# Kernel tuning notes

Measured on AMD Instinct MI355X. Metric: run time of the kernel, lower is better.

The kernel has to match this reference:

```python
import jax, jax.numpy as jnp
import numpy as np

LSH_NUM_PROJS = 7
BLOCK_SIZE = 256      # key block size
SAMPLE_SIZE = 256
B, H, N, D = 1, 32, 8192, 128


def _gray_perm(num_projs):
    # AngularLSH._unit_hamming_distance_array: Gray-code bucket permutation
    a = np.array([0, 1], dtype=np.int32)
    for _ in range(num_projs - 1):
        a = np.concatenate([a, np.flip(a) + a.shape[0]])
    return jnp.asarray(a)


def _lsh_hash(x, proj_dir, perm):
    # x: [B,H,N,D], proj_dir: [D,R] -> bucket ids [B,H,N]
    bits = jnp.einsum('bhnd,dr->bhnr', x, proj_dir) > 0
    enc = 2 ** jnp.arange(proj_dir.shape[-1], dtype=jnp.int32)
    bin_ids = jnp.sum(bits.astype(jnp.int32) * enc, axis=-1)
    return perm[bin_ids]


def _attn_lse(q, k, v, scale, bias=None):
    # exact attention returning output and log-sum-exp of scaled scores
    s = jnp.einsum('...qd,...kd->...qk', q, k) * scale
    if bias is not None:
        s = s + bias
    m = jnp.max(s, axis=-1, keepdims=True)
    p = jnp.exp(s - m)
    denom = jnp.sum(p, axis=-1, keepdims=True)
    attn = jnp.einsum('...qk,...kd->...qd', p, v) / denom
    lse = m + jnp.log(denom)  # [..., q, 1]
    return attn, lse


def _take(x, idx):
    # gather along the sequence axis (dim 2); idx: [B,H,M]
    return jnp.take_along_axis(x, idx[..., None], axis=2)


def hyper_attention(q, k, v, proj_dir, sampled_set):
    b, h, n, d = q.shape
    scale = d ** -0.5
    perm = _gray_perm(LSH_NUM_PROJS)
    # 1) sortLSH: sort q and k by angular-LSH bucket (stable)
    q_idx = jnp.argsort(_lsh_hash(q, proj_dir, perm), axis=2)
    k_idx = jnp.argsort(_lsh_hash(k, proj_dir, perm), axis=2)
    q_idx_inv = jnp.argsort(q_idx, axis=2)
    q_s = _take(q, q_idx)
    k_s = _take(k, k_idx)
    v_s = _take(v, k_idx)
    nb = n // BLOCK_SIZE          # number of key blocks
    qbs = n // nb                 # query block size
    # block-diagonal exact attention in sorted order
    qb = q_s.reshape(b, h, nb, qbs, d)
    kb = k_s.reshape(b, h, nb, BLOCK_SIZE, d)
    vb = v_s.reshape(b, h, nb, BLOCK_SIZE, d)
    attn_blk, lse_blk = _attn_lse(qb, kb, vb, scale)
    attn_blk = attn_blk.reshape(b, h, n, d)
    lse_blk = lse_blk.reshape(b, h, n, 1)
    attn_blk = _take(attn_blk, q_idx_inv)
    lse_blk = _take(lse_blk, q_idx_inv)
    # 2) residual: uniform sampling of keys (indices into sorted key order)
    s_size = sampled_set.shape[-1]
    k_sub = _take(k_s, sampled_set)   # [B,H,S,D]
    v_sub = _take(v_s, sampled_set)
    # mask out samples falling in the query's own diagonal block
    same_block = (jnp.arange(n)[None, None, :, None] // qbs) == (sampled_set[:, :, None, :] // BLOCK_SIZE)
    bias = jnp.where(same_block, jnp.finfo(q.dtype).min, 0.0).astype(q.dtype)
    attn_res, lse_res = _attn_lse(q_s, k_sub, v_sub, scale, bias=bias)
    lse_res = lse_res + jnp.log(n / s_size)  # importance weight n_key/sample_size
    attn_res = _take(attn_res, q_idx_inv)
    lse_res = _take(lse_res, q_idx_inv)
    # 3) combine estimators: softmax-weighted average in log space
    lse = jnp.logaddexp(lse_blk, lse_res)
    return jnp.exp(lse_blk - lse) * attn_blk + jnp.exp(lse_res - lse) * attn_res


def setup_inputs() -> dict:
    key = jax.random.key(0)
    k1, k2, k3, k4, k5 = jax.random.split(key, 5)
    return {
        'queries': jax.random.normal(k1, (B, H, N, D), dtype=jnp.float32),
        'keys': jax.random.normal(k2, (B, H, N, D), dtype=jnp.float32),
        'vals': jax.random.normal(k3, (B, H, N, D), dtype=jnp.float32),
        'proj_dir': jax.random.normal(k4, (D, LSH_NUM_PROJS), dtype=jnp.float32),
        'sampled_set': jax.random.randint(k5, (B, H, SAMPLE_SIZE), 0, N),
    }


def reference(queries, keys, vals, proj_dir, sampled_set):
    return hyper_attention(queries, keys, vals, proj_dir, sampled_set)
```

## Files before the change

kernel.cpp:

```cpp
#include <hip/hip_runtime.h>
#include <hip/hip_bf16.h>
#include <math.h>

#define Hh 32
#define Nseq 8192
#define Dh 128
#define NBd 32
#define BLKSZ 256
#define SAMP 256
#define KVT 512
#define CHK 64
#define NCH 8
#define LOG32 3.4657359027997265f
#define SCALE 0.088388347648318447f
#define SKW 136

typedef float f32x4 __attribute__((ext_vector_type(4)));
typedef unsigned ui32x4 __attribute__((ext_vector_type(4)));
typedef __bf16 bf16x8 __attribute__((ext_vector_type(8)));

__device__ __forceinline__ f32x4 mfma16(bf16x8 a, bf16x8 b, f32x4 c) {
  return __builtin_amdgcn_mfma_f32_16x16x32_bf16(a, b, c, 0, 0, 0);
}

__device__ __forceinline__ bf16x8 cvt8(const float* __restrict__ p) {
  float4 a = ((const float4*)p)[0];
  float4 b = ((const float4*)p)[1];
  bf16x8 r;
  r[0] = (__bf16)a.x; r[1] = (__bf16)a.y; r[2] = (__bf16)a.z; r[3] = (__bf16)a.w;
  r[4] = (__bf16)b.x; r[5] = (__bf16)b.y; r[6] = (__bf16)b.z; r[7] = (__bf16)b.w;
  return r;
}

__device__ __forceinline__ bf16x8 cvt8v(float4 a, float4 b) {
  bf16x8 r;
  r[0] = (__bf16)a.x; r[1] = (__bf16)a.y; r[2] = (__bf16)a.z; r[3] = (__bf16)a.w;
  r[4] = (__bf16)b.x; r[5] = (__bf16)b.y; r[6] = (__bf16)b.z; r[7] = (__bf16)b.w;
  return r;
}

__device__ __forceinline__ unsigned pack2(float a, float b, float& ra, float& rb) {
  __bf16 ba = (__bf16)a, bb = (__bf16)b;
  ra = (float)ba; rb = (float)bb;
  return ((unsigned)__builtin_bit_cast(unsigned short, bb) << 16) |
         (unsigned)__builtin_bit_cast(unsigned short, ba);
}

__global__ __launch_bounds__(256) void lsh_hash_kernel(
    const float* __restrict__ q, const float* __restrict__ k,
    const float* __restrict__ proj, int* __restrict__ buckets) {
  int row = blockIdx.x * 256 + threadIdx.x;
  const float* x = ((row >> 18) ? k : q) + (size_t)(row & (Hh * Nseq - 1)) * Dh;
  double acc[7] = {0, 0, 0, 0, 0, 0, 0};
#pragma unroll 8
  for (int d0 = 0; d0 < Dh; d0 += 4) {
    float4 xv = *(const float4*)(x + d0);
    double x0 = (double)xv.x, x1 = (double)xv.y, x2 = (double)xv.z, x3 = (double)xv.w;
#pragma unroll
    for (int j = 0; j < 7; j++) {
      acc[j] = fma(x0, (double)proj[(d0 + 0) * 7 + j], acc[j]);
      acc[j] = fma(x1, (double)proj[(d0 + 1) * 7 + j], acc[j]);
      acc[j] = fma(x2, (double)proj[(d0 + 2) * 7 + j], acc[j]);
      acc[j] = fma(x3, (double)proj[(d0 + 3) * 7 + j], acc[j]);
    }
  }
  int bin = 0;
#pragma unroll
  for (int j = 0; j < 7; j++) bin |= (acc[j] > 0.0 ? 1 : 0) << j;
  buckets[row] = bin ^ (bin >> 1);
}

__global__ __launch_bounds__(64) void bucket_sort_kernel(
    const int* __restrict__ buckets, int* __restrict__ idx) {
  __shared__ unsigned hist[64][128];
  int t = threadIdx.x;
  int base = blockIdx.x * Nseq;
  for (int b = 0; b < 128; b++) hist[t][b] = 0;
  __syncthreads();
  for (int i = 0; i < 128; i++) {
    int b = buckets[base + t * 128 + i];
    hist[t][b]++;
  }
  __syncthreads();
  int b0 = 2 * t, b1 = 2 * t + 1;
  unsigned tot0 = 0, tot1 = 0;
  for (int tt = 0; tt < 64; tt++) { unsigned h = hist[tt][b0]; hist[tt][b0] = tot0; tot0 += h; }
  for (int tt = 0; tt < 64; tt++) { unsigned h = hist[tt][b1]; hist[tt][b1] = tot1; tot1 += h; }
  unsigned pair = tot0 + tot1;
  unsigned scan = pair;
  for (int s = 1; s < 64; s <<= 1) {
    unsigned u = __shfl_up(scan, s);
    if (t >= s) scan += u;
  }
  unsigned start0 = scan - pair;
  unsigned start1 = start0 + tot0;
  __syncthreads();
  for (int tt = 0; tt < 64; tt++) { hist[tt][b0] += start0; hist[tt][b1] += start1; }
  __syncthreads();
  for (int i = 0; i < 128; i++) {
    int gi = t * 128 + i;
    int b = buckets[base + gi];
    unsigned pos = hist[t][b]++;
    idx[base + pos] = gi;
  }
}

__global__ __launch_bounds__(512, 2) void hyper_attn_kernel(
    const float* __restrict__ q, const float* __restrict__ k, const float* __restrict__ v,
    const int* __restrict__ sampled, const int* __restrict__ q_idx,
    const int* __restrict__ k_idx, float* __restrict__ out) {
  __shared__ int s_orig[KVT];
  __shared__ __attribute__((aligned(16))) float s_add[KVT];
  __shared__ __attribute__((aligned(16))) __bf16 s_k[2][CHK][SKW];
  __shared__ __attribute__((aligned(16))) __bf16 s_vt[2][Dh][72];

  const int c = blockIdx.x, bh = blockIdx.y;
  const int tid = threadIdx.x;
  const int w = tid >> 6, l = tid & 63;
  const int l4 = l >> 4, lm = l & 15;
  const int jk = tid >> 3, pk = tid & 7;

  {
    int jj = tid;
    if (jj < BLKSZ) {
      s_orig[jj] = k_idx[bh * Nseq + c * BLKSZ + jj];
      s_add[jj] = 0.0f;
    } else {
      int sp = sampled[bh * SAMP + (jj - BLKSZ)];
      s_orig[jj] = k_idx[bh * Nseq + sp];
      s_add[jj] = ((sp >> 8) == c) ? -1e38f : LOG32;
    }
  }

  bf16x8 qf[2][4];
  const int* qi = q_idx + bh * Nseq + c * BLKSZ + w * 32;
#pragma unroll
  for (int rt = 0; rt < 2; rt++) {
    int orig = qi[rt * 16 + lm];
    const float* qp = q + ((size_t)bh * Nseq + orig) * Dh + l4 * 8;
#pragma unroll
    for (int dc = 0; dc < 4; dc++) qf[rt][dc] = cvt8(qp + dc * 32);
  }

  f32x4 O[2][8];
  float mrow[2] = {-INFINITY, -INFINITY};
  float lsum[2] = {0.f, 0.f};
#pragma unroll
  for (int rt = 0; rt < 2; rt++)
#pragma unroll
    for (int dt = 0; dt < 8; dt++) { O[rt][dt][0]=0.f; O[rt][dt][1]=0.f; O[rt][dt][2]=0.f; O[rt][dt][3]=0.f; }

  __syncthreads();

  {
    int origk = s_orig[jk];
    const float* kp = k + ((size_t)bh * Nseq + origk) * Dh + pk * 16;
    *(bf16x8*)&s_k[0][jk][pk * 16]     = cvt8(kp);
    *(bf16x8*)&s_k[0][jk][pk * 16 + 8] = cvt8(kp + 8);
    int origv = s_orig[l];
    const float* vp = v + ((size_t)bh * Nseq + origv) * Dh + w * 16;
    float4 A = ((const float4*)vp)[0], B = ((const float4*)vp)[1];
    float4 C = ((const float4*)vp)[2], Dv = ((const float4*)vp)[3];
    float tmp[16] = {A.x,A.y,A.z,A.w,B.x,B.y,B.z,B.w,C.x,C.y,C.z,C.w,Dv.x,Dv.y,Dv.z,Dv.w};
#pragma unroll
    for (int dd = 0; dd < 16; dd++) s_vt[0][w * 16 + dd][l] = (__bf16)tmp[dd];
  }
  __syncthreads();

  const int laneA = lm + 32 * (l4 & 1);
  const bool hi = (l4 >> 1) & 1;

  for (int ch = 0; ch < NCH; ch++) {
    const int cur = ch & 1;
    const bool pf = (ch + 1 < NCH);

    float4 kA, kB, kC, kD, vA, vB, vC, vD;
    if (pf) {
      int origk = s_orig[(ch + 1) * CHK + jk];
      const float4* kp = (const float4*)(k + ((size_t)bh * Nseq + origk) * Dh + pk * 16);
      kA = kp[0]; kB = kp[1]; kC = kp[2]; kD = kp[3];
      int origv = s_orig[(ch + 1) * CHK + l];
      const float4* vp = (const float4*)(v + ((size_t)bh * Nseq + origv) * Dh + w * 16);
      vA = vp[0]; vB = vp[1]; vC = vp[2]; vD = vp[3];
    }

    float sc[2][4][4];
#pragma unroll
    for (int ct = 0; ct < 4; ct++) {
      f32x4 acc0, acc1;
      acc0[0]=0.f;acc0[1]=0.f;acc0[2]=0.f;acc0[3]=0.f;
      acc1[0]=0.f;acc1[1]=0.f;acc1[2]=0.f;acc1[3]=0.f;
#pragma unroll
      for (int dc = 0; dc < 4; dc++) {
        bf16x8 kf = *(const bf16x8*)&s_k[cur][ct * 16 + lm][dc * 32 + l4 * 8];
        acc0 = mfma16(kf, qf[0][dc], acc0);
        acc1 = mfma16(kf, qf[1][dc], acc1);
      }
      f32x4 addv = *(const f32x4*)&s_add[ch * CHK + ct * 16 + l4 * 4];
#pragma unroll
      for (int r = 0; r < 4; r++) {
        sc[0][ct][r] = acc0[r] * SCALE + addv[r];
        sc[1][ct][r] = acc1[r] * SCALE + addv[r];
      }
    }

    unsigned q01[2][4], q23[2][4];
#pragma unroll
    for (int rt = 0; rt < 2; rt++) {
      float mc = sc[rt][0][0];
#pragma unroll
      for (int ct = 0; ct < 4; ct++)
#pragma unroll
        for (int r = 0; r < 4; r++) mc = fmaxf(mc, sc[rt][ct][r]);
      mc = fmaxf(mc, __shfl_xor(mc, 16));
      mc = fmaxf(mc, __shfl_xor(mc, 32));
      float mn = fmaxf(mrow[rt], mc);
      float alpha = __expf(mrow[rt] - mn);
      mrow[rt] = mn;
      f32x4 aO;
#pragma unroll
      for (int r = 0; r < 4; r++) aO[r] = __shfl(alpha, l4 * 4 + r);
#pragma unroll
      for (int dt = 0; dt < 8; dt++) O[rt][dt] *= aO;
      float rsum = 0.f;
#pragma unroll
      for (int ct = 0; ct < 4; ct++) {
        float p0 = __expf(sc[rt][ct][0] - mn);
        float p1 = __expf(sc[rt][ct][1] - mn);
        float p2 = __expf(sc[rt][ct][2] - mn);
        float p3 = __expf(sc[rt][ct][3] - mn);
        float ra, rb, rc, rd;
        q01[rt][ct] = pack2(p0, p1, ra, rb);
        q23[rt][ct] = pack2(p2, p3, rc, rd);
        rsum += (ra + rb) + (rc + rd);
      }
      rsum += __shfl_xor(rsum, 16);
      rsum += __shfl_xor(rsum, 32);
      lsum[rt] = lsum[rt] * alpha + rsum;
    }

    if (pf) {
      *(bf16x8*)&s_k[cur ^ 1][jk][pk * 16]     = cvt8v(kA, kB);
      *(bf16x8*)&s_k[cur ^ 1][jk][pk * 16 + 8] = cvt8v(kC, kD);
      float tmp[16] = {vA.x,vA.y,vA.z,vA.w,vB.x,vB.y,vB.z,vB.w,
                       vC.x,vC.y,vC.z,vC.w,vD.x,vD.y,vD.z,vD.w};
#pragma unroll
      for (int dd = 0; dd < 16; dd++) s_vt[cur ^ 1][w * 16 + dd][l] = (__bf16)tmp[dd];
    }

#pragma unroll
    for (int kc = 0; kc < 2; kc++) {
      bf16x8 pa[2];
#pragma unroll
      for (int rt = 0; rt < 2; rt++) {
        unsigned a0 = __shfl((int)q01[rt][2 * kc],     laneA);
        unsigned b0 = __shfl((int)q01[rt][2 * kc + 1], laneA);
        unsigned a1 = __shfl((int)q23[rt][2 * kc],     laneA);
        unsigned b1 = __shfl((int)q23[rt][2 * kc + 1], laneA);
        unsigned a2 = __shfl((int)q01[rt][2 * kc],     laneA + 16);
        unsigned b2 = __shfl((int)q01[rt][2 * kc + 1], laneA + 16);
        unsigned a3 = __shfl((int)q23[rt][2 * kc],     laneA + 16);
        unsigned b3 = __shfl((int)q23[rt][2 * kc + 1], laneA + 16);
        ui32x4 pw;
        pw[0] = hi ? b0 : a0;
        pw[1] = hi ? b1 : a1;
        pw[2] = hi ? b2 : a2;
        pw[3] = hi ? b3 : a3;
        pa[rt] = __builtin_bit_cast(bf16x8, pw);
      }
#pragma unroll
      for (int dt = 0; dt < 8; dt++) {
        bf16x8 vb = *(const bf16x8*)&s_vt[cur][dt * 16 + lm][kc * 32 + l4 * 8];
        O[0][dt] = mfma16(pa[0], vb, O[0][dt]);
        O[1][dt] = mfma16(pa[1], vb, O[1][dt]);
      }
    }
    __syncthreads();
  }

#pragma unroll
  for (int rt = 0; rt < 2; rt++) {
    float inv = 1.0f / lsum[rt];
    f32x4 invr;
#pragma unroll
    for (int r = 0; r < 4; r++) invr[r] = __shfl(inv, l4 * 4 + r);
    int orow[4];
#pragma unroll
    for (int r = 0; r < 4; r++)
      orow[r] = q_idx[bh * Nseq + c * BLKSZ + w * 32 + rt * 16 + l4 * 4 + r];
#pragma unroll
    for (int r = 0; r < 4; r++) {
      float* op = out + ((size_t)bh * Nseq + orow[r]) * Dh + lm;
#pragma unroll
      for (int dt = 0; dt < 8; dt++) op[dt * 16] = O[rt][dt][r] * invr[r];
    }
  }
}

extern "C" void kernel_launch(void* const* d_in, const int* in_sizes, int n_in,
                              void* d_out, int out_size, void* d_ws, size_t ws_size,
                              hipStream_t stream) {
  const float* q    = (const float*)d_in[0];
  const float* k    = (const float*)d_in[1];
  const float* v    = (const float*)d_in[2];
  const float* proj = (const float*)d_in[3];
  const int* samp   = (const int*)d_in[4];
  float* out = (float*)d_out;

  int* buckets = (int*)d_ws;
  int* idx = buckets + 2 * Hh * Nseq;

  lsh_hash_kernel<<<(2 * Hh * Nseq) / 256, 256, 0, stream>>>(q, k, proj, buckets);
  bucket_sort_kernel<<<2 * Hh, 64, 0, stream>>>(buckets, idx);
  hyper_attn_kernel<<<dim3(NBd, Hh), 512, 0, stream>>>(
      q, k, v, samp, idx , idx + Hh * Nseq , out);
}
```

Measured before the change: 274.2 us.

## Remap V transpose stores to paired 32-bit writes and swizzle block order

```diff
diff --git a/kernel.cpp b/kernel.cpp
--- a/kernel.cpp
+++ b/kernel.cpp
@@ -39,6 +39,12 @@
   return r;
 }
 
+__device__ __forceinline__ unsigned packv(float a, float b) {
+  __bf16 ba = (__bf16)a, bb = (__bf16)b;
+  return ((unsigned)__builtin_bit_cast(unsigned short, bb) << 16) |
+         (unsigned)__builtin_bit_cast(unsigned short, ba);
+}
+
 __device__ __forceinline__ unsigned pack2(float a, float b, float& ra, float& rb) {
   __bf16 ba = (__bf16)a, bb = (__bf16)b;
   ra = (float)ba; rb = (float)bb;
@@ -114,11 +120,13 @@
   __shared__ __attribute__((aligned(16))) __bf16 s_k[2][CHK][SKW];
   __shared__ __attribute__((aligned(16))) __bf16 s_vt[2][Dh][72];
 
-  const int c = blockIdx.x, bh = blockIdx.y;
+  const int swz = ((blockIdx.x & 7) << 7) | (blockIdx.x >> 3);
+  const int c = swz & 31, bh = swz >> 5;
   const int tid = threadIdx.x;
   const int w = tid >> 6, l = tid & 63;
   const int l4 = l >> 4, lm = l & 15;
   const int jk = tid >> 3, pk = tid & 7;
+  const int kb = (tid & 31) * 2, dg = tid >> 5;
 
   {
     int jj = tid;
@@ -157,13 +165,15 @@
     const float* kp = k + ((size_t)bh * Nseq + origk) * Dh + pk * 16;
     *(bf16x8*)&s_k[0][jk][pk * 16]     = cvt8(kp);
     *(bf16x8*)&s_k[0][jk][pk * 16 + 8] = cvt8(kp + 8);
-    int origv = s_orig[l];
-    const float* vp = v + ((size_t)bh * Nseq + origv) * Dh + w * 16;
-    float4 A = ((const float4*)vp)[0], B = ((const float4*)vp)[1];
-    float4 C = ((const float4*)vp)[2], Dv = ((const float4*)vp)[3];
-    float tmp[16] = {A.x,A.y,A.z,A.w,B.x,B.y,B.z,B.w,C.x,C.y,C.z,C.w,Dv.x,Dv.y,Dv.z,Dv.w};
-#pragma unroll
-    for (int dd = 0; dd < 16; dd++) s_vt[0][w * 16 + dd][l] = (__bf16)tmp[dd];
+    int ra = s_orig[kb], rb = s_orig[kb + 1];
+    const float4* va = (const float4*)(v + ((size_t)bh * Nseq + ra) * Dh + dg * 8);
+    const float4* vb = (const float4*)(v + ((size_t)bh * Nseq + rb) * Dh + dg * 8);
+    float4 A0 = va[0], A1 = va[1], B0 = vb[0], B1 = vb[1];
+    float ta[8] = {A0.x,A0.y,A0.z,A0.w,A1.x,A1.y,A1.z,A1.w};
+    float tb[8] = {B0.x,B0.y,B0.z,B0.w,B1.x,B1.y,B1.z,B1.w};
+#pragma unroll
+    for (int dd = 0; dd < 8; dd++)
+      *(unsigned*)&s_vt[0][dg * 8 + dd][kb] = packv(ta[dd], tb[dd]);
   }
   __syncthreads();
 
@@ -174,15 +184,17 @@
     const int cur = ch & 1;
     const bool pf = (ch + 1 < NCH);
 
-    float4 kA, kB, kC, kD, vA, vB, vC, vD;
+    float4 kA, kB, kC, kD, vA0, vA1, vB0, vB1;
     if (pf) {
       int origk = s_orig[(ch + 1) * CHK + jk];
       const float4* kp = (const float4*)(k + ((size_t)bh * Nseq + origk) * Dh + pk * 16);
       kA = kp[0]; kB = kp[1]; kC = kp[2]; kD = kp[3];
-      int origv = s_orig[(ch + 1) * CHK + l];
-      const float4* vp = (const float4*)(v + ((size_t)bh * Nseq + origv) * Dh + w * 16);
-      vA = vp[0]; vB = vp[1]; vC = vp[2]; vD = vp[3];
-    }
+      int ra = s_orig[(ch + 1) * CHK + kb], rb = s_orig[(ch + 1) * CHK + kb + 1];
+      const float4* va = (const float4*)(v + ((size_t)bh * Nseq + ra) * Dh + dg * 8);
+      const float4* vb = (const float4*)(v + ((size_t)bh * Nseq + rb) * Dh + dg * 8);
+      vA0 = va[0]; vA1 = va[1]; vB0 = vb[0]; vB1 = vb[1];
+    }
+    __builtin_amdgcn_sched_barrier(0);
 
     float sc[2][4][4];
 #pragma unroll
@@ -242,10 +254,11 @@
     if (pf) {
       *(bf16x8*)&s_k[cur ^ 1][jk][pk * 16]     = cvt8v(kA, kB);
       *(bf16x8*)&s_k[cur ^ 1][jk][pk * 16 + 8] = cvt8v(kC, kD);
-      float tmp[16] = {vA.x,vA.y,vA.z,vA.w,vB.x,vB.y,vB.z,vB.w,
-                       vC.x,vC.y,vC.z,vC.w,vD.x,vD.y,vD.z,vD.w};
-#pragma unroll
-      for (int dd = 0; dd < 16; dd++) s_vt[cur ^ 1][w * 16 + dd][l] = (__bf16)tmp[dd];
+      float ta[8] = {vA0.x,vA0.y,vA0.z,vA0.w,vA1.x,vA1.y,vA1.z,vA1.w};
+      float tb[8] = {vB0.x,vB0.y,vB0.z,vB0.w,vB1.x,vB1.y,vB1.z,vB1.w};
+#pragma unroll
+      for (int dd = 0; dd < 8; dd++)
+        *(unsigned*)&s_vt[cur ^ 1][dg * 8 + dd][kb] = packv(ta[dd], tb[dd]);
     }
 
 #pragma unroll
@@ -312,6 +325,6 @@
 
   lsh_hash_kernel<<<(2 * Hh * Nseq) / 256, 256, 0, stream>>>(q, k, proj, buckets);
   bucket_sort_kernel<<<2 * Hh, 64, 0, stream>>>(buckets, idx);
-  hyper_attn_kernel<<<dim3(NBd, Hh), 512, 0, stream>>>(
+  hyper_attn_kernel<<<NBd * Hh, 512, 0, stream>>>(
       q, k, v, samp, idx , idx + Hh * Nseq , out);
 }
```

After: 279.3 us. About the same (+1.9%).

## Split block and residual attention into two kernels with shared sampled KV

Applied to the files above, without the earlier changes.

```diff
diff --git a/kernel.cpp b/kernel.cpp
--- a/kernel.cpp
+++ b/kernel.cpp
@@ -8,12 +8,11 @@
 #define NBd 32
 #define BLKSZ 256
 #define SAMP 256
-#define KVT 512
 #define CHK 64
-#define NCH 8
 #define LOG32 3.4657359027997265f
 #define SCALE 0.088388347648318447f
 #define SKW 136
+#define SVB 264
 
 typedef float f32x4 __attribute__((ext_vector_type(4)));
 typedef unsigned ui32x4 __attribute__((ext_vector_type(4)));
@@ -105,12 +104,11 @@
   }
 }
 
-__global__ __launch_bounds__(512, 2) void hyper_attn_kernel(
+__global__ __launch_bounds__(512, 2) void hyper_attn_blk_kernel(
     const float* __restrict__ q, const float* __restrict__ k, const float* __restrict__ v,
-    const int* __restrict__ sampled, const int* __restrict__ q_idx,
-    const int* __restrict__ k_idx, float* __restrict__ out) {
-  __shared__ int s_orig[KVT];
-  __shared__ __attribute__((aligned(16))) float s_add[KVT];
+    const int* __restrict__ q_idx, const int* __restrict__ k_idx,
+    float* __restrict__ out, float* __restrict__ lse_ws) {
+  __shared__ int s_orig[BLKSZ];
   __shared__ __attribute__((aligned(16))) __bf16 s_k[2][CHK][SKW];
   __shared__ __attribute__((aligned(16))) __bf16 s_vt[2][Dh][72];
 
@@ -120,17 +118,7 @@
   const int l4 = l >> 4, lm = l & 15;
   const int jk = tid >> 3, pk = tid & 7;
 
-  {
-    int jj = tid;
-    if (jj < BLKSZ) {
-      s_orig[jj] = k_idx[bh * Nseq + c * BLKSZ + jj];
-      s_add[jj] = 0.0f;
-    } else {
-      int sp = sampled[bh * SAMP + (jj - BLKSZ)];
-      s_orig[jj] = k_idx[bh * Nseq + sp];
-      s_add[jj] = ((sp >> 8) == c) ? -1e38f : LOG32;
-    }
-  }
+  if (tid < BLKSZ) s_orig[tid] = k_idx[bh * Nseq + c * BLKSZ + tid];
 
   bf16x8 qf[2][4];
   const int* qi = q_idx + bh * Nseq + c * BLKSZ + w * 32;
@@ -170,9 +158,9 @@
   const int laneA = lm + 32 * (l4 & 1);
   const bool hi = (l4 >> 1) & 1;
 
-  for (int ch = 0; ch < NCH; ch++) {
+  for (int ch = 0; ch < 4; ch++) {
     const int cur = ch & 1;
-    const bool pf = (ch + 1 < NCH);
+    const bool pf = (ch + 1 < 4);
 
     float4 kA, kB, kC, kD, vA, vB, vC, vD;
     if (pf) {
@@ -196,11 +184,10 @@
         acc0 = mfma16(kf, qf[0][dc], acc0);
         acc1 = mfma16(kf, qf[1][dc], acc1);
       }
-      f32x4 addv = *(const f32x4*)&s_add[ch * CHK + ct * 16 + l4 * 4];
 #pragma unroll
       for (int r = 0; r < 4; r++) {
-        sc[0][ct][r] = acc0[r] * SCALE + addv[r];
-        sc[1][ct][r] = acc1[r] * SCALE + addv[r];
+        sc[0][ct][r] = acc0[r] * SCALE;
+        sc[1][ct][r] = acc1[r] * SCALE;
       }
     }
 
@@ -242,10 +229,10 @@
     if (pf) {
       *(bf16x8*)&s_k[cur ^ 1][jk][pk * 16]     = cvt8v(kA, kB);
       *(bf16x8*)&s_k[cur ^ 1][jk][pk * 16 + 8] = cvt8v(kC, kD);
-      float tmp[16] = {vA.x,vA.y,vA.z,vA.w,vB.x,vB.y,vB.z,vB.w,
-                       vC.x,vC.y,vC.z,vC.w,vD.x,vD.y,vD.z,vD.w};
-#pragma unroll
-      for (int dd = 0; dd < 16; dd++) s_vt[cur ^ 1][w * 16 + dd][l] = (__bf16)tmp[dd];
+      float ta[16] = {vA.x,vA.y,vA.z,vA.w,vB.x,vB.y,vB.z,vB.w,
+                      vC.x,vC.y,vC.z,vC.w,vD.x,vD.y,vD.z,vD.w};
+#pragma unroll
+      for (int dd = 0; dd < 16; dd++) s_vt[cur ^ 1][w * 16 + dd][l] = (__bf16)ta[dd];
     }
 
 #pragma unroll
@@ -294,6 +281,182 @@
 #pragma unroll
       for (int dt = 0; dt < 8; dt++) op[dt * 16] = O[rt][dt][r] * invr[r];
     }
+    if (l4 == 0) {
+      int orow0 = q_idx[bh * Nseq + c * BLKSZ + w * 32 + rt * 16 + lm];
+      lse_ws[bh * Nseq + orow0] = mrow[rt] + __logf(lsum[rt]);
+    }
+  }
+}
+
+__global__ __launch_bounds__(512, 1) void hyper_attn_res_kernel(
+    const float* __restrict__ q, const float* __restrict__ k, const float* __restrict__ v,
+    const int* __restrict__ sampled, const int* __restrict__ q_idx,
+    const int* __restrict__ k_idx, const float* __restrict__ lse_ws,
+    float* __restrict__ out) {
+  __shared__ int s_sp[SAMP];
+  __shared__ __attribute__((aligned(16))) __bf16 s_k[SAMP][SKW];
+  __shared__ __attribute__((aligned(16))) __bf16 s_vt[Dh][SVB];
+
+  const int bh = blockIdx.x >> 3, oct = blockIdx.x & 7;
+  const int tid = threadIdx.x;
+  const int w = tid >> 6, l = tid & 63;
+  const int l4 = l >> 4, lm = l & 15;
+  const int jk = tid >> 3, pk = tid & 7;
+
+  if (tid < SAMP) s_sp[tid] = sampled[bh * SAMP + tid];
+
+#pragma unroll
+  for (int ps = 0; ps < 4; ps++) {
+    int key = ps * 64 + jk;
+    int sp = sampled[bh * SAMP + key];
+    int orig = k_idx[bh * Nseq + sp];
+    const float4* kp = (const float4*)(k + ((size_t)bh * Nseq + orig) * Dh + pk * 16);
+    *(bf16x8*)&s_k[key][pk * 16]     = cvt8v(kp[0], kp[1]);
+    *(bf16x8*)&s_k[key][pk * 16 + 8] = cvt8v(kp[2], kp[3]);
+  }
+#pragma unroll
+  for (int ps = 0; ps < 4; ps++) {
+    int key = ps * 64 + l;
+    int sp = sampled[bh * SAMP + key];
+    int orig = k_idx[bh * Nseq + sp];
+    const float4* vp = (const float4*)(v + ((size_t)bh * Nseq + orig) * Dh + w * 16);
+    float4 A = vp[0], B = vp[1], C = vp[2], Dv = vp[3];
+    float tmp[16] = {A.x,A.y,A.z,A.w,B.x,B.y,B.z,B.w,C.x,C.y,C.z,C.w,Dv.x,Dv.y,Dv.z,Dv.w};
+#pragma unroll
+    for (int dd = 0; dd < 16; dd++) s_vt[w * 16 + dd][key] = (__bf16)tmp[dd];
+  }
+  __syncthreads();
+
+  const int laneA = lm + 32 * (l4 & 1);
+  const bool hi = (l4 >> 1) & 1;
+
+  for (int t = 0; t < 4; t++) {
+    const int rowb = oct * 1024 + w * 128 + t * 32;
+    const int c_tile = rowb >> 8;
+
+    bf16x8 qf[2][4];
+#pragma unroll
+    for (int rt = 0; rt < 2; rt++) {
+      int orig = q_idx[bh * Nseq + rowb + rt * 16 + lm];
+      const float* qp = q + ((size_t)bh * Nseq + orig) * Dh + l4 * 8;
+#pragma unroll
+      for (int dc = 0; dc < 4; dc++) qf[rt][dc] = cvt8(qp + dc * 32);
+    }
+
+    f32x4 O[2][8];
+    float mrow[2] = {-INFINITY, -INFINITY};
+    float lsum[2] = {0.f, 0.f};
+#pragma unroll
+    for (int rt = 0; rt < 2; rt++)
+#pragma unroll
+      for (int dt = 0; dt < 8; dt++) { O[rt][dt][0]=0.f; O[rt][dt][1]=0.f; O[rt][dt][2]=0.f; O[rt][dt][3]=0.f; }
+
+    for (int ch = 0; ch < 4; ch++) {
+      float sc[2][4][4];
+#pragma unroll
+      for (int ct = 0; ct < 4; ct++) {
+        f32x4 acc0, acc1;
+        acc0[0]=0.f;acc0[1]=0.f;acc0[2]=0.f;acc0[3]=0.f;
+        acc1[0]=0.f;acc1[1]=0.f;acc1[2]=0.f;acc1[3]=0.f;
+#pragma unroll
+        for (int dc = 0; dc < 4; dc++) {
+          bf16x8 kf = *(const bf16x8*)&s_k[ch * 64 + ct * 16 + lm][dc * 32 + l4 * 8];
+          acc0 = mfma16(kf, qf[0][dc], acc0);
+          acc1 = mfma16(kf, qf[1][dc], acc1);
+        }
+        ui32x4 spv = *(const ui32x4*)&s_sp[ch * 64 + ct * 16 + l4 * 4];
+#pragma unroll
+        for (int r = 0; r < 4; r++) {
+          float add = ((((int)spv[r]) >> 8) == c_tile) ? -1e38f : LOG32;
+          sc[0][ct][r] = acc0[r] * SCALE + add;
+          sc[1][ct][r] = acc1[r] * SCALE + add;
+        }
+      }
+
+      unsigned q01[2][4], q23[2][4];
+#pragma unroll
+      for (int rt = 0; rt < 2; rt++) {
+        float mc = sc[rt][0][0];
+#pragma unroll
+        for (int ct = 0; ct < 4; ct++)
+#pragma unroll
+          for (int r = 0; r < 4; r++) mc = fmaxf(mc, sc[rt][ct][r]);
+        mc = fmaxf(mc, __shfl_xor(mc, 16));
+        mc = fmaxf(mc, __shfl_xor(mc, 32));
+        float mn = fmaxf(mrow[rt], mc);
+        float alpha = __expf(mrow[rt] - mn);
+        mrow[rt] = mn;
+        f32x4 aO;
+#pragma unroll
+        for (int r = 0; r < 4; r++) aO[r] = __shfl(alpha, l4 * 4 + r);
+#pragma unroll
+        for (int dt = 0; dt < 8; dt++) O[rt][dt] *= aO;
+        float rsum = 0.f;
+#pragma unroll
+        for (int ct = 0; ct < 4; ct++) {
+          float p0 = __expf(sc[rt][ct][0] - mn);
+          float p1 = __expf(sc[rt][ct][1] - mn);
+          float p2 = __expf(sc[rt][ct][2] - mn);
+          float p3 = __expf(sc[rt][ct][3] - mn);
+          float ra, rb, rc, rd;
+          q01[rt][ct] = pack2(p0, p1, ra, rb);
+          q23[rt][ct] = pack2(p2, p3, rc, rd);
+          rsum += (ra + rb) + (rc + rd);
+        }
+        rsum += __shfl_xor(rsum, 16);
+        rsum += __shfl_xor(rsum, 32);
+        lsum[rt] = lsum[rt] * alpha + rsum;
+      }
+
+#pragma unroll
+      for (int kc = 0; kc < 2; kc++) {
+        bf16x8 pa[2];
+#pragma unroll
+        for (int rt = 0; rt < 2; rt++) {
+          unsigned a0 = __shfl((int)q01[rt][2 * kc],     laneA);
+          unsigned b0 = __shfl((int)q01[rt][2 * kc + 1], laneA);
+          unsigned a1 = __shfl((int)q23[rt][2 * kc],     laneA);
+          unsigned b1 = __shfl((int)q23[rt][2 * kc + 1], laneA);
+          unsigned a2 = __shfl((int)q01[rt][2 * kc],     laneA + 16);
+          unsigned b2 = __shfl((int)q01[rt][2 * kc + 1], laneA + 16);
+          unsigned a3 = __shfl((int)q23[rt][2 * kc],     laneA + 16);
+          unsigned b3 = __shfl((int)q23[rt][2 * kc + 1], laneA + 16);
+          ui32x4 pw;
+          pw[0] = hi ? b0 : a0;
+          pw[1] = hi ? b1 : a1;
+          pw[2] = hi ? b2 : a2;
+          pw[3] = hi ? b3 : a3;
+          pa[rt] = __builtin_bit_cast(bf16x8, pw);
+        }
+#pragma unroll
+        for (int dt = 0; dt < 8; dt++) {
+          bf16x8 vb = *(const bf16x8*)&s_vt[dt * 16 + lm][ch * 64 + kc * 32 + l4 * 8];
+          O[0][dt] = mfma16(pa[0], vb, O[0][dt]);
+          O[1][dt] = mfma16(pa[1], vb, O[1][dt]);
+        }
+      }
+    }
+
+#pragma unroll
+    for (int rt = 0; rt < 2; rt++) {
+      float lse_r = mrow[rt] + __logf(lsum[rt]);
+      float inv = 1.0f / lsum[rt];
+#pragma unroll
+      for (int r = 0; r < 4; r++) {
+        float lrr  = __shfl(lse_r, l4 * 4 + r);
+        float invr = __shfl(inv,   l4 * 4 + r);
+        int orow = q_idx[bh * Nseq + rowb + rt * 16 + l4 * 4 + r];
+        float lb = lse_ws[bh * Nseq + orow];
+        float m2 = fmaxf(lb, lrr);
+        float wb = __expf(lb - m2), wr = __expf(lrr - m2);
+        float sw = 1.0f / (wb + wr);
+        wb *= sw; wr *= sw;
+        float* op = out + ((size_t)bh * Nseq + orow) * Dh + lm;
+#pragma unroll
+        for (int dt = 0; dt < 8; dt++)
+          op[dt * 16] = wb * op[dt * 16] + wr * (O[rt][dt][r] * invr);
+      }
+    }
   }
 }
 
@@ -309,9 +472,12 @@
 
   int* buckets = (int*)d_ws;
   int* idx = buckets + 2 * Hh * Nseq;
+  float* lse_ws = (float*)buckets;
 
   lsh_hash_kernel<<<(2 * Hh * Nseq) / 256, 256, 0, stream>>>(q, k, proj, buckets);
   bucket_sort_kernel<<<2 * Hh, 64, 0, stream>>>(buckets, idx);
-  hyper_attn_kernel<<<dim3(NBd, Hh), 512, 0, stream>>>(
-      q, k, v, samp, idx , idx + Hh * Nseq , out);
-}
+  hyper_attn_blk_kernel<<<dim3(NBd, Hh), 512, 0, stream>>>(
+      q, k, v, idx , idx + Hh * Nseq , out, lse_ws);
+  hyper_attn_res_kernel<<<8 * Hh, 512, 0, stream>>>(
+      q, k, v, samp, idx , idx + Hh * Nseq , lse_ws, out);
+}
```

Result: slower. 326.3 us (+19.0%).

## Precompute sampled K/V in bf16 with pre-transposed V in a separate kernel

Applied to the files above, without the earlier changes.

```diff
diff --git a/kernel.cpp b/kernel.cpp
--- a/kernel.cpp
+++ b/kernel.cpp
@@ -8,12 +8,12 @@
 #define NBd 32
 #define BLKSZ 256
 #define SAMP 256
-#define KVT 512
 #define CHK 64
 #define NCH 8
 #define LOG32 3.4657359027997265f
 #define SCALE 0.088388347648318447f
 #define SKW 136
+#define SVW 72
 
 typedef float f32x4 __attribute__((ext_vector_type(4)));
 typedef unsigned ui32x4 __attribute__((ext_vector_type(4)));
@@ -105,30 +105,68 @@
   }
 }
 
+__global__ __launch_bounds__(256) void permute_samp_kernel(
+    const float* __restrict__ k, const float* __restrict__ v,
+    const int* __restrict__ k_idx, const int* __restrict__ sampled,
+    __bf16* __restrict__ K_sp, __bf16* __restrict__ V_sp) {
+  __shared__ __attribute__((aligned(16))) __bf16 s_t[Dh][SVW];
+  const int tile = blockIdx.x, bh = blockIdx.y;
+  const int t = threadIdx.x;
+  const int j = t >> 2, seg = (t & 3) * 32;
+  const int dpos = tile * 64 + j;
+  const int sp = sampled[bh * SAMP + dpos];
+  const int orig = k_idx[bh * Nseq + sp];
+  {
+    const float4* kp = (const float4*)(k + ((size_t)bh * Nseq + orig) * Dh + seg);
+    __bf16* dst = K_sp + ((size_t)bh * SAMP + dpos) * Dh + seg;
+#pragma unroll
+    for (int i = 0; i < 4; i++) *(bf16x8*)(dst + i * 8) = cvt8v(kp[2 * i], kp[2 * i + 1]);
+  }
+  {
+    const float4* vp = (const float4*)(v + ((size_t)bh * Nseq + orig) * Dh + seg);
+#pragma unroll
+    for (int i = 0; i < 8; i++) {
+      float4 a = vp[i];
+      s_t[seg + i * 4 + 0][j] = (__bf16)a.x;
+      s_t[seg + i * 4 + 1][j] = (__bf16)a.y;
+      s_t[seg + i * 4 + 2][j] = (__bf16)a.z;
+      s_t[seg + i * 4 + 3][j] = (__bf16)a.w;
+    }
+  }
+  __syncthreads();
+  {
+    int d = t >> 1, half = (t & 1) * 32;
+    __bf16* dst = V_sp + ((size_t)(bh * Dh + d)) * SAMP + tile * 64 + half;
+    const __bf16* srcp = &s_t[d][half];
+#pragma unroll
+    for (int i = 0; i < 4; i++) *(ui32x4*)(dst + i * 8) = *(const ui32x4*)(srcp + i * 8);
+  }
+}
+
 __global__ __launch_bounds__(512, 2) void hyper_attn_kernel(
     const float* __restrict__ q, const float* __restrict__ k, const float* __restrict__ v,
+    const __bf16* __restrict__ K_sp, const __bf16* __restrict__ V_sp,
     const int* __restrict__ sampled, const int* __restrict__ q_idx,
     const int* __restrict__ k_idx, float* __restrict__ out) {
-  __shared__ int s_orig[KVT];
-  __shared__ __attribute__((aligned(16))) float s_add[KVT];
+  __shared__ int s_orig[BLKSZ];
+  __shared__ __attribute__((aligned(16))) float s_add[SAMP];
   __shared__ __attribute__((aligned(16))) __bf16 s_k[2][CHK][SKW];
-  __shared__ __attribute__((aligned(16))) __bf16 s_vt[2][Dh][72];
+  __shared__ __attribute__((aligned(16))) __bf16 s_vt[2][Dh][SVW];
 
   const int c = blockIdx.x, bh = blockIdx.y;
   const int tid = threadIdx.x;
   const int w = tid >> 6, l = tid & 63;
   const int l4 = l >> 4, lm = l & 15;
   const int jk = tid >> 3, pk = tid & 7;
+  const int dv = tid >> 2, ks = (tid & 3) * 16;
 
   {
     int jj = tid;
     if (jj < BLKSZ) {
       s_orig[jj] = k_idx[bh * Nseq + c * BLKSZ + jj];
-      s_add[jj] = 0.0f;
     } else {
       int sp = sampled[bh * SAMP + (jj - BLKSZ)];
-      s_orig[jj] = k_idx[bh * Nseq + sp];
-      s_add[jj] = ((sp >> 8) == c) ? -1e38f : LOG32;
+      s_add[jj - BLKSZ] = ((sp >> 8) == c) ? -1e38f : LOG32;
     }
   }
 
@@ -172,16 +210,24 @@
 
   for (int ch = 0; ch < NCH; ch++) {
     const int cur = ch & 1;
-    const bool pf = (ch + 1 < NCH);
+    const int cn = ch + 1;
+    const bool pfg = (cn < 4);
+    const bool pfc = (cn >= 4 && cn < NCH);
 
     float4 kA, kB, kC, kD, vA, vB, vC, vD;
-    if (pf) {
-      int origk = s_orig[(ch + 1) * CHK + jk];
+    ui32x4 ksA, ksB, vsA, vsB;
+    if (pfg) {
+      int origk = s_orig[cn * CHK + jk];
       const float4* kp = (const float4*)(k + ((size_t)bh * Nseq + origk) * Dh + pk * 16);
       kA = kp[0]; kB = kp[1]; kC = kp[2]; kD = kp[3];
-      int origv = s_orig[(ch + 1) * CHK + l];
+      int origv = s_orig[cn * CHK + l];
       const float4* vp = (const float4*)(v + ((size_t)bh * Nseq + origv) * Dh + w * 16);
       vA = vp[0]; vB = vp[1]; vC = vp[2]; vD = vp[3];
+    } else if (pfc) {
+      const __bf16* kp = K_sp + ((size_t)(bh * SAMP + (cn - 4) * CHK + jk)) * Dh + pk * 16;
+      ksA = *(const ui32x4*)kp; ksB = *(const ui32x4*)(kp + 8);
+      const __bf16* vp = V_sp + ((size_t)(bh * Dh + dv)) * SAMP + (cn - 4) * CHK + ks;
+      vsA = *(const ui32x4*)vp; vsB = *(const ui32x4*)(vp + 8);
     }
 
     float sc[2][4][4];
@@ -196,7 +242,9 @@
         acc0 = mfma16(kf, qf[0][dc], acc0);
         acc1 = mfma16(kf, qf[1][dc], acc1);
       }
-      f32x4 addv = *(const f32x4*)&s_add[ch * CHK + ct * 16 + l4 * 4];
+      f32x4 addv;
+      if (ch < 4) { addv[0]=0.f; addv[1]=0.f; addv[2]=0.f; addv[3]=0.f; }
+      else addv = *(const f32x4*)&s_add[(ch - 4) * CHK + ct * 16 + l4 * 4];
 #pragma unroll
       for (int r = 0; r < 4; r++) {
         sc[0][ct][r] = acc0[r] * SCALE + addv[r];
@@ -239,13 +287,18 @@
       lsum[rt] = lsum[rt] * alpha + rsum;
     }
 
-    if (pf) {
+    if (pfg) {
       *(bf16x8*)&s_k[cur ^ 1][jk][pk * 16]     = cvt8v(kA, kB);
       *(bf16x8*)&s_k[cur ^ 1][jk][pk * 16 + 8] = cvt8v(kC, kD);
-      float tmp[16] = {vA.x,vA.y,vA.z,vA.w,vB.x,vB.y,vB.z,vB.w,
-                       vC.x,vC.y,vC.z,vC.w,vD.x,vD.y,vD.z,vD.w};
-#pragma unroll
-      for (int dd = 0; dd < 16; dd++) s_vt[cur ^ 1][w * 16 + dd][l] = (__bf16)tmp[dd];
+      float ta[16] = {vA.x,vA.y,vA.z,vA.w,vB.x,vB.y,vB.z,vB.w,
+                      vC.x,vC.y,vC.z,vC.w,vD.x,vD.y,vD.z,vD.w};
+#pragma unroll
+      for (int dd = 0; dd < 16; dd++) s_vt[cur ^ 1][w * 16 + dd][l] = (__bf16)ta[dd];
+    } else if (pfc) {
+      *(ui32x4*)&s_k[cur ^ 1][jk][pk * 16]     = ksA;
+      *(ui32x4*)&s_k[cur ^ 1][jk][pk * 16 + 8] = ksB;
+      *(ui32x4*)&s_vt[cur ^ 1][dv][ks]     = vsA;
+      *(ui32x4*)&s_vt[cur ^ 1][dv][ks + 8] = vsB;
     }
 
 #pragma unroll
@@ -284,13 +337,10 @@
     f32x4 invr;
 #pragma unroll
     for (int r = 0; r < 4; r++) invr[r] = __shfl(inv, l4 * 4 + r);
-    int orow[4];
-#pragma unroll
-    for (int r = 0; r < 4; r++)
-      orow[r] = q_idx[bh * Nseq + c * BLKSZ + w * 32 + rt * 16 + l4 * 4 + r];
 #pragma unroll
     for (int r = 0; r < 4; r++) {
-      float* op = out + ((size_t)bh * Nseq + orow[r]) * Dh + lm;
+      int orow = q_idx[bh * Nseq + c * BLKSZ + w * 32 + rt * 16 + l4 * 4 + r];
+      float* op = out + ((size_t)bh * Nseq + orow) * Dh + lm;
 #pragma unroll
       for (int dt = 0; dt < 8; dt++) op[dt * 16] = O[rt][dt][r] * invr[r];
     }
@@ -309,9 +359,13 @@
 
   int* buckets = (int*)d_ws;
   int* idx = buckets + 2 * Hh * Nseq;
+  __bf16* K_sp = (__bf16*)(idx + 2 * Hh * Nseq);
+  __bf16* V_sp = K_sp + (size_t)Hh * SAMP * Dh;
 
   lsh_hash_kernel<<<(2 * Hh * Nseq) / 256, 256, 0, stream>>>(q, k, proj, buckets);
   bucket_sort_kernel<<<2 * Hh, 64, 0, stream>>>(buckets, idx);
+  permute_samp_kernel<<<dim3(4, Hh), 256, 0, stream>>>(
+      k, v, idx + Hh * Nseq , samp, K_sp, V_sp);
   hyper_attn_kernel<<<dim3(NBd, Hh), 512, 0, stream>>>(
-      q, k, v, samp, idx , idx + Hh * Nseq , out);
-}
+      q, k, v, K_sp, V_sp, samp, idx , idx + Hh * Nseq , out);
+}
```

Result: no change. 271.1 us (-1.1%).
